# Kernel optimization log

Measured on AMD Instinct MI355X. Metric: run time of the kernel, lower is better.

Reference implementation:

```python
import jax, jax.numpy as jnp
import numpy as np

N = 100000  # nodes (in_features)
D = 32      # out_features
E = 1600000 # edges


def setup_inputs() -> dict:
    key = jax.random.key(0)
    k1, k2, k3, k4, k5 = jax.random.split(key, 5)
    edge_row = jax.random.randint(k1, (E,), 0, N, dtype=jnp.int64)
    edge_col = jax.random.randint(k2, (E,), 0, N, dtype=jnp.int64)
    edge_val = jax.random.uniform(k3, (E,), dtype=jnp.float32)
    weight = jax.random.normal(k4, (N, D), dtype=jnp.float32)
    bias = jax.random.normal(k5, (D,), dtype=jnp.float32)
    return {"edge_row": edge_row, "edge_col": edge_col,
            "edge_val": edge_val, "weight": weight, "bias": bias}


def reference(edge_row, edge_col, edge_val, weight, bias):
    # out = adj @ weight + bias, adj given in COO form.
    # Gather weight rows per edge column, scale by edge value,
    # segment-sum into destination rows. [E, D] intermediate.
    contrib = edge_val[:, None] * jnp.take(weight, edge_col, axis=0)
    out = jax.ops.segment_sum(contrib, edge_row, num_segments=N)
    return out + bias
```

## Files before the change

### kernel.cpp

```cpp
#include <hip/hip_runtime.h>


#define FEAT 32
#define LOG_RPB 7
#define RPB (1 << LOG_RPB)
#define COLBITS 17
#define CMASK ((1u << COLBITS) - 1)
#define BMAX 1024
#define PCHUNK 4096
#define PTHREADS 1024
#define EPT (PCHUNK / PTHREADS)
#define CAPB 2560
#define CAP_MAX 32


__global__ __launch_bounds__(256) void gnn_zero(
    int* __restrict__ cursor, int* __restrict__ scnt, int B) {
    int i = blockIdx.x * 256 + threadIdx.x;
    if (i < B) cursor[i] = 0;
    if (i == B) *scnt = 0;
}

__global__ __launch_bounds__(PTHREADS) void gnn_part(
    const int* __restrict__ edge_row,
    const int* __restrict__ edge_col,
    const float* __restrict__ edge_val,
    int* __restrict__ cursor,
    float2* __restrict__ parts,
    float4* __restrict__ spill,
    int* __restrict__ scnt,
    int num_edges, int B) {
    __shared__ float2 lrec[PCHUNK];
    __shared__ unsigned short lbkt[PCHUNK];
    __shared__ int st[BMAX];
    __shared__ int cur[BMAX];
    __shared__ int rb[BMAX];
    int t = threadIdx.x;
    for (int b = t; b < BMAX; b += PTHREADS) cur[b] = 0;
    __syncthreads();

    int e0 = blockIdx.x * PCHUNK;
    int cnt_chunk = num_edges - e0;
    if (cnt_chunk > PCHUNK) cnt_chunk = PCHUNK;

    int  r[EPT], c[EPT];
    float vv[EPT];
    int ebase = e0 + 4 * t;
    if (ebase + 3 < num_edges) {
        int4  r4 = *(const int4*)(edge_row + ebase);
        int4  c4 = *(const int4*)(edge_col + ebase);
        float4 v4 = *(const float4*)(edge_val + ebase);
        r[0] = r4.x; r[1] = r4.y; r[2] = r4.z; r[3] = r4.w;
        c[0] = c4.x; c[1] = c4.y; c[2] = c4.z; c[3] = c4.w;
        vv[0] = v4.x; vv[1] = v4.y; vv[2] = v4.z; vv[3] = v4.w;
    } else {
        #pragma unroll
        for (int k = 0; k < EPT; ++k) {
            int e = ebase + k;
            bool ok = e < num_edges;
            r[k]  = ok ? edge_row[e] : -1;
            c[k]  = ok ? edge_col[e] : 0;
            vv[k] = ok ? edge_val[e] : 0.f;
        }
    }
    #pragma unroll
    for (int k = 0; k < EPT; ++k)
        if (r[k] >= 0) atomicAdd(&cur[r[k] >> LOG_RPB], 1);
    __syncthreads();

    int v = (t < B) ? cur[t] : 0;
    st[t] = v;
    __syncthreads();
    for (int off = 1; off < BMAX; off <<= 1) {
        int u = (t >= off) ? st[t - off] : 0;
        __syncthreads();
        st[t] += u;
        __syncthreads();
    }
    st[t] -= v;
    if (t < B) {
        cur[t] = st[t];
        rb[t]  = v ? atomicAdd(&cursor[t], v) : 0;
    }
    __syncthreads();

    #pragma unroll
    for (int k = 0; k < EPT; ++k) {
        if (r[k] >= 0) {
            int bb = r[k] >> LOG_RPB;
            int slot = atomicAdd(&cur[bb], 1);
            unsigned pk = (unsigned)c[k] |
                          ((unsigned)(r[k] & (RPB - 1)) << COLBITS);
            lrec[slot] = make_float2(__uint_as_float(pk), vv[k]);
            lbkt[slot] = (unsigned short)bb;
        }
    }
    __syncthreads();

    for (int i = t; i < cnt_chunk; i += PTHREADS) {
        int bb = lbkt[i];
        float2 rec = lrec[i];
        int s = rb[bb] + (i - st[bb]);
        if (s < CAPB) {
            parts[(long long)bb * CAPB + s] = rec;
        } else {
            int si = atomicAdd(scnt, 1);
            unsigned pk = __float_as_uint(rec.x);
            spill[si] = make_float4(
                __uint_as_float((unsigned)(bb << LOG_RPB) + (pk >> COLBITS)),
                __uint_as_float(pk & CMASK), rec.y, 0.f);
        }
    }
}

__global__ __launch_bounds__(512) void gnn_accum(
    const float2* __restrict__ parts,
    const int* __restrict__ cursor,
    const float* __restrict__ weight,
    const float* __restrict__ bias,
    float* __restrict__ out,
    int n_nodes) {
    __shared__ float2 srec[CAPB];
    __shared__ int h[RPB];
    __shared__ int sc[RPB];
    __shared__ int rs[RPB + 1];
    __shared__ int cur[RPB];
    int b = blockIdx.x, t = threadIdx.x;
    int n = cursor[b];
    int m = n < CAPB ? n : CAPB;
    const float2* p = parts + (long long)b * CAPB;

    float2 rec[CAPB / 512];
    #pragma unroll
    for (int k = 0; k < CAPB / 512; ++k) {
        int idx = t + k * 512;
        rec[k] = (idx < m) ? p[idx] : make_float2(0.f, 0.f);
    }

    if (t < RPB) h[t] = 0;
    __syncthreads();
    #pragma unroll
    for (int k = 0; k < CAPB / 512; ++k) {
        int idx = t + k * 512;
        if (idx < m) {
            unsigned rl = (__float_as_uint(rec[k].x) >> COLBITS) & (RPB - 1);
            atomicAdd(&h[rl], 1);
        }
    }
    __syncthreads();

    if (t < RPB) sc[t] = h[t];
    __syncthreads();
    #pragma unroll
    for (int off = 1; off < RPB; off <<= 1) {
        int u = (t < RPB && t >= off) ? sc[t - off] : 0;
        __syncthreads();
        if (t < RPB) sc[t] += u;
        __syncthreads();
    }
    if (t < RPB) {
        rs[t + 1] = sc[t];
        cur[t] = sc[t] - h[t];
    }
    if (t == 0) rs[0] = 0;
    __syncthreads();

    #pragma unroll
    for (int k = 0; k < CAPB / 512; ++k) {
        int idx = t + k * 512;
        if (idx < m) {
            unsigned rl = (__float_as_uint(rec[k].x) >> COLBITS) & (RPB - 1);
            int slot = atomicAdd(&cur[rl], 1);
            srec[slot] = rec[k];
        }
    }
    __syncthreads();

    int g = t >> 5;
    int f = t & 31;
    int row0 = b << LOG_RPB;
    float bf = bias[f];
    #pragma unroll 1
    for (int rr = 0; rr < 8; ++rr) {
        int rl = (g << 3) + rr;
        int s = rs[rl], e = rs[rl + 1];
        float acc = 0.f;
        for (int j = s; j < e; j += 8) {
            #pragma unroll
            for (int k = 0; k < 8; ++k) {
                int jj = j + k;
                bool ok = jj < e;
                float2 rc = srec[ok ? jj : s];
                unsigned cc = __float_as_uint(rc.x) & CMASK;
                float w = weight[cc * FEAT + f];
                acc += ok ? rc.y * w : 0.f;
            }
        }
        int rrow = row0 + rl;
        if (rrow < n_nodes)
            out[(long long)rrow * FEAT + f] = acc + bf;
    }
}

__global__ __launch_bounds__(256) void gnn_spill(
    const float4* __restrict__ spill,
    const int* __restrict__ scnt,
    const float* __restrict__ weight,
    float* __restrict__ out,
    int n_nodes) {
    int total = *scnt;
    int idx = (blockIdx.x * 256 + threadIdx.x) >> 5;
    int f = threadIdx.x & 31;
    int stride = (gridDim.x * 256) >> 5;
    for (; idx < total; idx += stride) {
        float4 s = spill[idx];
        int r = (int)__float_as_uint(s.x);
        int c = (int)__float_as_uint(s.y);
        if (r < n_nodes)
            atomicAdd(out + (long long)r * FEAT + f,
                      s.z * weight[(long long)c * FEAT + f]);
    }
}


__global__ __launch_bounds__(256) void gnn_init(
    const float* __restrict__ bias, float* __restrict__ out,
    int* __restrict__ cnt, int total4, int n_nodes) {
    int i = blockIdx.x * blockDim.x + threadIdx.x;
    if (i < total4) {
        float4 bb = ((const float4*)bias)[i & 7];
        ((float4*)out)[i] = bb;
    }
    if (i < n_nodes) cnt[i] = 0;
}

__global__ __launch_bounds__(256) void gnn_bin(
    const int* __restrict__ edge_row,
    const int* __restrict__ edge_col,
    const float* __restrict__ edge_val,
    const float* __restrict__ weight,
    float2* __restrict__ bins,
    int* __restrict__ cnt,
    float* __restrict__ out,
    int num_edges, int cap) {
    int e = blockIdx.x * blockDim.x + threadIdx.x;
    if (e >= num_edges) return;
    int r = edge_row[e];
    int c = edge_col[e];
    float v = edge_val[e];
    int slot = atomicAdd(&cnt[r], 1);
    if (slot < cap) {
        bins[(long long)r * cap + slot] = make_float2(__int_as_float(c), v);
    } else {
        const float* w = weight + (long long)c * FEAT;
        #pragma unroll
        for (int f = 0; f < FEAT; ++f)
            atomicAdd(out + (long long)r * FEAT + f, v * w[f]);
    }
}

__global__ __launch_bounds__(256) void gnn_gather(
    const float2* __restrict__ bins,
    const int* __restrict__ cnt,
    const float* __restrict__ weight,
    float* __restrict__ out,
    int n_nodes, int cap) {
    int g = (blockIdx.x * blockDim.x + threadIdx.x) >> 5;
    int f = threadIdx.x & (FEAT - 1);
    if (g >= n_nodes) return;
    int n = cnt[g];
    n = n < cap ? n : cap;
    const float2* b = bins + (long long)g * cap;
    float a0 = 0.f, a1 = 0.f, a2 = 0.f, a3 = 0.f;
    int j = 0;
    for (; j + 4 <= n; j += 4) {
        float2 e0 = b[j], e1 = b[j + 1], e2 = b[j + 2], e3 = b[j + 3];
        a0 += e0.y * weight[(long long)__float_as_int(e0.x) * FEAT + f];
        a1 += e1.y * weight[(long long)__float_as_int(e1.x) * FEAT + f];
        a2 += e2.y * weight[(long long)__float_as_int(e2.x) * FEAT + f];
        a3 += e3.y * weight[(long long)__float_as_int(e3.x) * FEAT + f];
    }
    for (; j < n; ++j) {
        float2 e0 = b[j];
        a0 += e0.y * weight[(long long)__float_as_int(e0.x) * FEAT + f];
    }
    out[(long long)g * FEAT + f] += (a0 + a1) + (a2 + a3);
}


__global__ __launch_bounds__(256) void gnn_init_out(
    const float* __restrict__ bias, float* __restrict__ out, int total) {
    int i = blockIdx.x * blockDim.x + threadIdx.x;
    if (i < total) out[i] = bias[i & (FEAT - 1)];
}

__global__ __launch_bounds__(256) void gnn_scatter(
    const int* __restrict__ edge_row,
    const int* __restrict__ edge_col,
    const float* __restrict__ edge_val,
    const float* __restrict__ weight,
    float* __restrict__ out,
    int num_edges) {
    long long t = (long long)blockIdx.x * blockDim.x + threadIdx.x;
    int e = (int)(t >> 5);
    int f = (int)(t & (FEAT - 1));
    if (e < num_edges) {
        int r = edge_row[e];
        int c = edge_col[e];
        atomicAdd(out + r * FEAT + f, edge_val[e] * weight[c * FEAT + f]);
    }
}

extern "C" void kernel_launch(void* const* d_in, const int* in_sizes, int n_in,
                              void* d_out, int out_size, void* d_ws, size_t ws_size,
                              hipStream_t stream) {
    const int*   edge_row = (const int*)d_in[0];
    const int*   edge_col = (const int*)d_in[1];
    const float* edge_val = (const float*)d_in[2];
    const float* weight   = (const float*)d_in[3];
    const float* bias     = (const float*)d_in[4];
    float* out = (float*)d_out;

    const int E = in_sizes[0];
    const int total = out_size;
    const int N = total / FEAT;
    const int B = (N + RPB - 1) >> LOG_RPB;

    auto align256 = [](size_t x) { return (x + 255) & ~(size_t)255; };
    size_t cursor_off = 0;
    size_t scnt_off   = align256(cursor_off + (size_t)B * sizeof(int));
    size_t spill_off  = align256(scnt_off + sizeof(int));
    size_t parts_off  = align256(spill_off + (size_t)E * sizeof(float4));
    size_t need_v6    = parts_off + (size_t)B * CAPB * sizeof(float2);

    if (B >= 1 && B <= BMAX && N <= (1 << COLBITS) && E > 0 && ws_size >= need_v6) {
        int*    cursor = (int*)((char*)d_ws + cursor_off);
        int*    scnt   = (int*)((char*)d_ws + scnt_off);
        float4* spill  = (float4*)((char*)d_ws + spill_off);
        float2* parts  = (float2*)((char*)d_ws + parts_off);

        gnn_zero<<<(B + 1 + 255) / 256, 256, 0, stream>>>(cursor, scnt, B);
        gnn_part<<<(E + PCHUNK - 1) / PCHUNK, PTHREADS, 0, stream>>>(
            edge_row, edge_col, edge_val, cursor, parts, spill, scnt, E, B);
        gnn_accum<<<B, 512, 0, stream>>>(
            parts, cursor, weight, bias, out, N);
        gnn_spill<<<32, 256, 0, stream>>>(spill, scnt, weight, out, N);
        return;
    }

    size_t cnt_bytes = align256((size_t)N * sizeof(int));
    long long cap_ll = 0;
    if (ws_size > cnt_bytes)
        cap_ll = (long long)((ws_size - cnt_bytes) / ((size_t)N * sizeof(float2)));
    int cap = (int)(cap_ll > CAP_MAX ? CAP_MAX : cap_ll);

    if (cap >= 16) {
        int* cnt = (int*)d_ws;
        float2* bins = (float2*)((char*)d_ws + cnt_bytes);
        int total4 = total / 4;
        int init_threads = total4 > N ? total4 : N;
        gnn_init<<<(init_threads + 255) / 256, 256, 0, stream>>>(
            bias, out, cnt, total4, N);
        gnn_bin<<<(E + 255) / 256, 256, 0, stream>>>(
            edge_row, edge_col, edge_val, weight, bins, cnt, out, E, cap);
        long long gthreads = (long long)N * FEAT;
        gnn_gather<<<(int)((gthreads + 255) / 256), 256, 0, stream>>>(
            bins, cnt, weight, out, N, cap);
    } else {
        gnn_init_out<<<(total + 255) / 256, 256, 0, stream>>>(bias, out, total);
        long long threads = (long long)E * FEAT;
        gnn_scatter<<<(int)((threads + 255) / 256), 256, 0, stream>>>(
            edge_row, edge_col, edge_val, weight, out, E);
    }
}
```

Measured before the change: 126.4 us.

## Reuse atomic slots to skip second counting pass and fold spill into accum

The partition and accumulate kernels now record the slot returned by the first shared-memory histogram atomic, then place records at prefix+slot. This removes the second round of shared atomics. The accumulate kernel replaces its 7-step block-wide scan with a single-wavefront shuffle scan over 128 bins, and batches 8 weight gathers ahead of the FMAs to raise memory-level parallelism. The separate spill kernel is removed: each row now scans the whole spill list itself. That saves a launch, but the cost becomes quadratic if spills are ever frequent.

```diff
diff --git a/kernel.cpp b/kernel.cpp
--- a/kernel.cpp
+++ b/kernel.cpp
@@ -32,18 +32,17 @@
     int num_edges, int B) {
     __shared__ float2 lrec[PCHUNK];
     __shared__ unsigned short lbkt[PCHUNK];
+    __shared__ int hcur[BMAX];
     __shared__ int st[BMAX];
-    __shared__ int cur[BMAX];
-    __shared__ int rb[BMAX];
     int t = threadIdx.x;
-    for (int b = t; b < BMAX; b += PTHREADS) cur[b] = 0;
+    hcur[t] = 0;
     __syncthreads();
 
     int e0 = blockIdx.x * PCHUNK;
     int cnt_chunk = num_edges - e0;
     if (cnt_chunk > PCHUNK) cnt_chunk = PCHUNK;
 
-    int  r[EPT], c[EPT];
+    int  r[EPT], c[EPT], bb[EPT], slot[EPT];
     float vv[EPT];
     int ebase = e0 + 4 * t;
     if (ebase + 3 < num_edges) {
@@ -64,50 +63,54 @@
         }
     }
     #pragma unroll
-    for (int k = 0; k < EPT; ++k)
-        if (r[k] >= 0) atomicAdd(&cur[r[k] >> LOG_RPB], 1);
-    __syncthreads();
-
-    int v = (t < B) ? cur[t] : 0;
+    for (int k = 0; k < EPT; ++k) {
+        if (r[k] >= 0) {
+            bb[k] = r[k] >> LOG_RPB;
+            slot[k] = atomicAdd(&hcur[bb[k]], 1);
+        }
+    }
+    __syncthreads();
+
+    int v = hcur[t];
     st[t] = v;
     __syncthreads();
+    #pragma unroll
     for (int off = 1; off < BMAX; off <<= 1) {
         int u = (t >= off) ? st[t - off] : 0;
         __syncthreads();
         st[t] += u;
         __syncthreads();
     }
-    st[t] -= v;
-    if (t < B) {
-        cur[t] = st[t];
-        rb[t]  = v ? atomicAdd(&cursor[t], v) : 0;
-    }
+    int ex = st[t] - v;
+    st[t] = ex;
+    int rbase = 0;
+    if (t < B && v) rbase = atomicAdd(&cursor[t], v);
+    hcur[t] = rbase;
     __syncthreads();
 
     #pragma unroll
     for (int k = 0; k < EPT; ++k) {
         if (r[k] >= 0) {
-            int bb = r[k] >> LOG_RPB;
-            int slot = atomicAdd(&cur[bb], 1);
+            int pos = st[bb[k]] + slot[k];
             unsigned pk = (unsigned)c[k] |
                           ((unsigned)(r[k] & (RPB - 1)) << COLBITS);
-            lrec[slot] = make_float2(__uint_as_float(pk), vv[k]);
-            lbkt[slot] = (unsigned short)bb;
+            lrec[pos] = make_float2(__uint_as_float(pk), vv[k]);
+            lbkt[pos] = (unsigned short)bb[k];
         }
     }
     __syncthreads();
 
     for (int i = t; i < cnt_chunk; i += PTHREADS) {
-        int bb = lbkt[i];
+        int b2 = lbkt[i];
         float2 rec = lrec[i];
-        int s = rb[bb] + (i - st[bb]);
+        int s = hcur[b2] + (i - st[b2]);
         if (s < CAPB) {
-            parts[(long long)bb * CAPB + s] = rec;
+            parts[(long long)b2 * CAPB + s] = rec;
         } else {
             int si = atomicAdd(scnt, 1);
             unsigned pk = __float_as_uint(rec.x);
             spill[si] = make_float4(
-                __uint_as_float((unsigned)(bb << LOG_RPB) + (pk >> COLBITS)),
+                __uint_as_float((unsigned)(b2 << LOG_RPB) + (pk >> COLBITS)),
                 __uint_as_float(pk & CMASK), rec.y, 0.f);
         }
     }
@@ -116,63 +119,58 @@
 __global__ __launch_bounds__(512) void gnn_accum(
     const float2* __restrict__ parts,
     const int* __restrict__ cursor,
+    const int* __restrict__ scnt,
+    const float4* __restrict__ spill,
     const float* __restrict__ weight,
     const float* __restrict__ bias,
     float* __restrict__ out,
     int n_nodes) {
     __shared__ float2 srec[CAPB];
     __shared__ int h[RPB];
-    __shared__ int sc[RPB];
     __shared__ int rs[RPB + 1];
-    __shared__ int cur[RPB];
     int b = blockIdx.x, t = threadIdx.x;
     int n = cursor[b];
+    int nspill = *scnt;
     int m = n < CAPB ? n : CAPB;
     const float2* p = parts + (long long)b * CAPB;
 
     float2 rec[CAPB / 512];
+    int rl[CAPB / 512], slot[CAPB / 512];
+    if (t < RPB) h[t] = 0;
+    __syncthreads();
     #pragma unroll
     for (int k = 0; k < CAPB / 512; ++k) {
         int idx = t + k * 512;
-        rec[k] = (idx < m) ? p[idx] : make_float2(0.f, 0.f);
-    }
-
-    if (t < RPB) h[t] = 0;
-    __syncthreads();
+        bool ok = idx < m;
+        rec[k] = ok ? p[idx] : make_float2(0.f, 0.f);
+        if (ok) {
+            rl[k] = (int)((__float_as_uint(rec[k].x) >> COLBITS) & (RPB - 1));
+            slot[k] = atomicAdd(&h[rl[k]], 1);
+        }
+    }
+    __syncthreads();
+
+    if (t < 64) {
+        int a  = h[2 * t];
+        int c2 = h[2 * t + 1];
+        int pr = a + c2;
+        int x = pr;
+        #pragma unroll
+        for (int off = 1; off < 64; off <<= 1) {
+            int y = __shfl_up(x, off);
+            if (t >= off) x += y;
+        }
+        int exc = x - pr;
+        rs[2 * t] = exc;
+        rs[2 * t + 1] = exc + a;
+        if (t == 63) rs[RPB] = x;
+    }
+    __syncthreads();
+
     #pragma unroll
     for (int k = 0; k < CAPB / 512; ++k) {
         int idx = t + k * 512;
-        if (idx < m) {
-            unsigned rl = (__float_as_uint(rec[k].x) >> COLBITS) & (RPB - 1);
-            atomicAdd(&h[rl], 1);
-        }
-    }
-    __syncthreads();
-
-    if (t < RPB) sc[t] = h[t];
-    __syncthreads();
-    #pragma unroll
-    for (int off = 1; off < RPB; off <<= 1) {
-        int u = (t < RPB && t >= off) ? sc[t - off] : 0;
-        __syncthreads();
-        if (t < RPB) sc[t] += u;
-        __syncthreads();
-    }
-    if (t < RPB) {
-        rs[t + 1] = sc[t];
-        cur[t] = sc[t] - h[t];
-    }
-    if (t == 0) rs[0] = 0;
-    __syncthreads();
-
-    #pragma unroll
-    for (int k = 0; k < CAPB / 512; ++k) {
-        int idx = t + k * 512;
-        if (idx < m) {
-            unsigned rl = (__float_as_uint(rec[k].x) >> COLBITS) & (RPB - 1);
-            int slot = atomicAdd(&cur[rl], 1);
-            srec[slot] = rec[k];
-        }
+        if (idx < m) srec[rs[rl[k]] + slot[k]] = rec[k];
     }
     __syncthreads();
 
@@ -182,43 +180,35 @@
     float bf = bias[f];
     #pragma unroll 1
     for (int rr = 0; rr < 8; ++rr) {
-        int rl = (g << 3) + rr;
-        int s = rs[rl], e = rs[rl + 1];
+        int rlc = (g << 3) + rr;
+        int s = rs[rlc], e = rs[rlc + 1];
         float acc = 0.f;
         for (int j = s; j < e; j += 8) {
+            float2 rc[8];
+            float w[8];
             #pragma unroll
             for (int k = 0; k < 8; ++k) {
                 int jj = j + k;
-                bool ok = jj < e;
-                float2 rc = srec[ok ? jj : s];
-                unsigned cc = __float_as_uint(rc.x) & CMASK;
-                float w = weight[cc * FEAT + f];
-                acc += ok ? rc.y * w : 0.f;
+                rc[k] = srec[jj < e ? jj : s];
             }
-        }
-        int rrow = row0 + rl;
+            #pragma unroll
+            for (int k = 0; k < 8; ++k)
+                w[k] = weight[(__float_as_uint(rc[k].x) & CMASK) * FEAT + f];
+            #pragma unroll
+            for (int k = 0; k < 8; ++k)
+                acc += (j + k < e) ? rc[k].y * w[k] : 0.f;
+        }
+        if (nspill > 0) {
+            for (int i = 0; i < nspill; ++i) {
+                float4 sp = spill[i];
+                if ((int)__float_as_uint(sp.x) == row0 + rlc)
+                    acc += sp.z *
+                           weight[__float_as_uint(sp.y) * FEAT + f];
+            }
+        }
+        int rrow = row0 + rlc;
         if (rrow < n_nodes)
             out[(long long)rrow * FEAT + f] = acc + bf;
-    }
-}
-
-__global__ __launch_bounds__(256) void gnn_spill(
-    const float4* __restrict__ spill,
-    const int* __restrict__ scnt,
-    const float* __restrict__ weight,
-    float* __restrict__ out,
-    int n_nodes) {
-    int total = *scnt;
-    int idx = (blockIdx.x * 256 + threadIdx.x) >> 5;
-    int f = threadIdx.x & 31;
-    int stride = (gridDim.x * 256) >> 5;
-    for (; idx < total; idx += stride) {
-        float4 s = spill[idx];
-        int r = (int)__float_as_uint(s.x);
-        int c = (int)__float_as_uint(s.y);
-        if (r < n_nodes)
-            atomicAdd(out + (long long)r * FEAT + f,
-                      s.z * weight[(long long)c * FEAT + f]);
     }
 }
 
@@ -331,9 +321,9 @@
     size_t scnt_off   = align256(cursor_off + (size_t)B * sizeof(int));
     size_t spill_off  = align256(scnt_off + sizeof(int));
     size_t parts_off  = align256(spill_off + (size_t)E * sizeof(float4));
-    size_t need_v6    = parts_off + (size_t)B * CAPB * sizeof(float2);
-
-    if (B >= 1 && B <= BMAX && N <= (1 << COLBITS) && E > 0 && ws_size >= need_v6) {
+    size_t need_v7    = parts_off + (size_t)B * CAPB * sizeof(float2);
+
+    if (B >= 1 && B <= BMAX && N <= (1 << COLBITS) && E > 0 && ws_size >= need_v7) {
         int*    cursor = (int*)((char*)d_ws + cursor_off);
         int*    scnt   = (int*)((char*)d_ws + scnt_off);
         float4* spill  = (float4*)((char*)d_ws + spill_off);
@@ -343,8 +333,7 @@
         gnn_part<<<(E + PCHUNK - 1) / PCHUNK, PTHREADS, 0, stream>>>(
             edge_row, edge_col, edge_val, cursor, parts, spill, scnt, E, B);
         gnn_accum<<<B, 512, 0, stream>>>(
-            parts, cursor, weight, bias, out, N);
-        gnn_spill<<<32, 256, 0, stream>>>(spill, scnt, weight, out, N);
+            parts, cursor, scnt, spill, weight, bias, out, N);
         return;
     }
 
```

After: 125.5 us. No clear change (-0.7%).
